# Optimization experiments

Hardware: AMD Instinct MI355X
Metric: run time of the kernel (lower is better)

## Reference

```python
import jax, jax.numpy as jnp
import numpy as np

N_QUBITS = 4
N_LAYERS = 2
_I2 = jnp.eye(2, dtype=jnp.complex64)
_X = jnp.array([[0.0, 1.0], [1.0, 0.0]], dtype=jnp.complex64)


def _apply_1q_batched(state, U, wire):
    # state: [B,2,2,2,2] complex, U: [B,2,2] (per-sample gate)
    s = jnp.moveaxis(state, 1 + wire, -1)
    s = jnp.einsum('bij,b...j->b...i', U, s)
    return jnp.moveaxis(s, -1, 1 + wire)


def _apply_1q(state, U, wire):
    # shared 2x2 gate on `wire`
    s = jnp.moveaxis(state, 1 + wire, -1)
    s = jnp.einsum('ij,...j->...i', U, s)
    return jnp.moveaxis(s, -1, 1 + wire)


def _apply_cnot(state, c, t):
    s = jnp.moveaxis(state, (1 + c, 1 + t), (-2, -1))  # [...,2(ctrl),2(tgt)]
    s = jnp.stack([s[..., 0, :], s[..., 1, ::-1]], axis=-2)  # flip target if ctrl=1
    return jnp.moveaxis(s, (-2, -1), (1 + c, 1 + t))


def _rot_matrix(phi, theta, omega):
    # qml.Rot = RZ(omega) @ RY(theta) @ RZ(phi)
    c, s = jnp.cos(theta / 2), jnp.sin(theta / 2)
    ep = jnp.exp(-0.5j * (phi + omega))  # e^{-i(phi+omega)/2}
    em = jnp.exp(-0.5j * (phi - omega))  # e^{-i(phi-omega)/2}
    return jnp.stack([
        jnp.stack([ep * c, -jnp.conj(em) * s]),
        jnp.stack([em * s, jnp.conj(ep) * c]),
    ]).astype(jnp.complex64)


def _circuit(angles, weights):
    # angles: [B, 4] real; weights: [2, 4, 3] real -> [B, 4] PauliZ expvals
    B = angles.shape[0]
    state = jnp.zeros((B,) + (2,) * N_QUBITS, jnp.complex64)
    state = state.at[(slice(None),) + (0,) * N_QUBITS].set(1.0)  # |0000>
    # AngleEmbedding (rotation='X'): RX(angle_w) on wire w, batched over samples
    for w in range(N_QUBITS):
        half = angles[:, w] / 2
        c, s = jnp.cos(half), jnp.sin(half)
        U = c[:, None, None] * _I2 - 1j * s[:, None, None] * _X  # [B,2,2]
        state = _apply_1q_batched(state, U, w)
    # StronglyEntanglingLayers: Rot on each wire, then ring of CNOTs with range r
    for l in range(N_LAYERS):
        for w in range(N_QUBITS):
            U = _rot_matrix(weights[l, w, 0], weights[l, w, 1], weights[l, w, 2])
            state = _apply_1q(state, U, w)
        r = (l % (N_QUBITS - 1)) + 1  # PennyLane default ranges
        for w in range(N_QUBITS):
            state = _apply_cnot(state, w, (w + r) % N_QUBITS)
    probs = state.real ** 2 + state.imag ** 2  # [B,2,2,2,2]
    z = []
    for w in range(N_QUBITS):
        other = tuple(a for a in range(1, N_QUBITS + 1) if a != 1 + w)
        p = probs.sum(other)  # [B,2]
        z.append(p[:, 0] - p[:, 1])
    return jnp.stack(z, axis=-1)  # [B,4]


def setup_inputs() -> dict:
    key = jax.random.key(0)
    ks = jax.random.split(key, 6)
    B, D_IN, D_OUT, NQ = 65536, 512, 512, N_QUBITS
    x = jax.random.normal(ks[0], (B, D_IN), jnp.float32)
    pre_W = jax.random.normal(ks[1], (NQ, D_IN), jnp.float32) / np.sqrt(D_IN)
    pre_b = jax.random.normal(ks[2], (NQ,), jnp.float32) * 0.05
    weights = jax.random.uniform(ks[3], (N_LAYERS, NQ, 3), jnp.float32) * (2 * np.pi)
    post_W = jax.random.normal(ks[4], (D_OUT, NQ), jnp.float32) / np.sqrt(NQ)
    post_b = jax.random.normal(ks[5], (D_OUT,), jnp.float32) * 0.05
    return {"x": x, "pre_W": pre_W, "pre_b": pre_b, "weights": weights,
            "post_W": post_W, "post_b": post_b}


def reference(x, pre_W, pre_b, weights, post_W, post_b):
    angles = jnp.tanh(x @ pre_W.T + pre_b) * jnp.pi  # [B,4]
    q = _circuit(angles, weights)                    # [B,4]
    return q @ post_W.T + post_b                     # [B,512]
```

## Files before the change

kernel.cpp:

```cpp
#include <hip/hip_runtime.h>
#include <math.h>

#define PI_F 3.14159265358979323846f


typedef float floatx4 __attribute__((ext_vector_type(4)));

static __device__ __forceinline__ void nt_store4(float* p, floatx4 v)
{
    __builtin_nontemporal_store(v, reinterpret_cast<floatx4*>(p));
}

static __device__ __forceinline__ float fast_tanh(float a)
{
    a = fminf(fmaxf(a, -15.f), 15.f);
    const float e = __expf(2.f * a);
    return (e - 1.f) / (e + 1.f);
}

template<int WIRE>
__device__ __forceinline__ void apply1q(float* sr, float* si,
    float u00r, float u00i, float u01r, float u01i,
    float u10r, float u10i, float u11r, float u11i)
{
    constexpr int st = 1 << (3 - WIRE);
#pragma unroll
    for (int i = 0; i < 16; ++i) {
        if (i & st) continue;
        const int j = i | st;
        const float r0 = sr[i], m0 = si[i], r1 = sr[j], m1 = si[j];
        sr[i] = u00r * r0 - u00i * m0 + u01r * r1 - u01i * m1;
        si[i] = u00r * m0 + u00i * r0 + u01r * m1 + u01i * r1;
        sr[j] = u10r * r0 - u10i * m0 + u11r * r1 - u11i * m1;
        si[j] = u10r * m0 + u10i * r0 + u11r * m1 + u11i * r1;
    }
}

template<int CW, int TW>
__device__ __forceinline__ void cnot(float* sr, float* si)
{
    constexpr int cb = 1 << (3 - CW), tb = 1 << (3 - TW);
#pragma unroll
    for (int i = 0; i < 16; ++i) {
        if ((i & cb) && !(i & tb)) {
            const int j = i | tb;
            float t;
            t = sr[i]; sr[i] = sr[j]; sr[j] = t;
            t = si[i]; si[i] = si[j]; si[j] = t;
        }
    }
}

#define APPLY_FAST(L, W) { \
    const float ph = wts[((L) * 4 + (W)) * 3 + 0]; \
    const float th = wts[((L) * 4 + (W)) * 3 + 1]; \
    const float om = wts[((L) * 4 + (W)) * 3 + 2]; \
    const float s_  = __sinf(0.5f * th),        c_  = __cosf(0.5f * th); \
    const float sp_ = __sinf(0.5f * (ph + om)), cp_ = __cosf(0.5f * (ph + om)); \
    const float sq_ = __sinf(0.5f * (ph - om)), cq_ = __cosf(0.5f * (ph - om)); \
    apply1q<W>(sr, si, cp_ * c_, -sp_ * c_, -cq_ * s_, -sq_ * s_, \
                       cq_ * s_, -sq_ * s_, cp_ * c_,  sp_ * c_); }

__global__ __launch_bounds__(256) void k_fused(
    const float* __restrict__ x,
    const float* __restrict__ preW,
    const float* __restrict__ preb,
    const float* __restrict__ wts,
    const float* __restrict__ postW,
    const float* __restrict__ postb,
    float* __restrict__ out, int B)
{
    const int lane  = threadIdx.x & 63;
    const int wid   = threadIdx.x >> 6;
    const int base  = blockIdx.x * 64;
    const int wbase = base + wid * 16;
    if (base >= B) return;

    __shared__ float4 angLds[64];

    float4 wA[4], wB[4];
#pragma unroll
    for (int w = 0; w < 4; ++w) {
        wA[w] = *reinterpret_cast<const float4*>(preW + w * 512 + lane * 4);
        wB[w] = *reinterpret_cast<const float4*>(preW + w * 512 + 256 + lane * 4);
    }
    const float4 pb = *reinterpret_cast<const float4*>(preb);

#pragma unroll
    for (int p = 0; p < 4; ++p) {
        const int b0 = wbase + p * 4;

        float4 xa[4], xb[4];
#pragma unroll
        for (int t = 0; t < 4; ++t) {
            const float* xr = x + (size_t)(b0 + t) * 512;
            xa[t] = *reinterpret_cast<const float4*>(xr + lane * 4);
            xb[t] = *reinterpret_cast<const float4*>(xr + 256 + lane * 4);
        }

        float acc[4][4];
#pragma unroll
        for (int t = 0; t < 4; ++t) {
#pragma unroll
            for (int w = 0; w < 4; ++w) {
                acc[t][w] = xa[t].x * wA[w].x + xa[t].y * wA[w].y + xa[t].z * wA[w].z + xa[t].w * wA[w].w
                          + xb[t].x * wB[w].x + xb[t].y * wB[w].y + xb[t].z * wB[w].z + xb[t].w * wB[w].w;
            }
        }

        float v[4];
#pragma unroll
        for (int t = 0; t < 4; ++t) {
            float a01 = (lane & 1) ? acc[t][1] : acc[t][0];
            float b01 = (lane & 1) ? acc[t][0] : acc[t][1];
            a01 += __shfl_xor(b01, 1, 64);
            float a23 = (lane & 1) ? acc[t][3] : acc[t][2];
            float b23 = (lane & 1) ? acc[t][2] : acc[t][3];
            a23 += __shfl_xor(b23, 1, 64);
            const float vv = (lane & 2) ? a23 : a01;
            const float uu = (lane & 2) ? a01 : a23;
            v[t] = vv + __shfl_xor(uu, 2, 64);
        }
        float c01 = (lane & 4) ? v[1] : v[0];
        float d01 = (lane & 4) ? v[0] : v[1];
        c01 += __shfl_xor(d01, 4, 64);
        float c23 = (lane & 4) ? v[3] : v[2];
        float d23 = (lane & 4) ? v[2] : v[3];
        c23 += __shfl_xor(d23, 4, 64);
        float m = (lane & 8) ? c23 : c01;
        float n = (lane & 8) ? c01 : c23;
        m += __shfl_xor(n, 8, 64);
        m += __shfl_xor(m, 16, 64);
        m += __shfl_xor(m, 32, 64);

        const float pb01 = (lane & 1) ? pb.y : pb.x;
        const float pb23 = (lane & 1) ? pb.w : pb.z;
        const float pbv  = (lane & 2) ? pb23 : pb01;
        const float angv = fast_tanh(m + pbv) * PI_F;

        if (lane < 16) {
            float* arow = reinterpret_cast<float*>(&angLds[wid * 16 + p * 4 + (lane >> 2)]);
            arow[lane & 3] = angv;
        }
    }

    __syncthreads();

    const int sid = lane >> 2;
    const float4 ang = angLds[wid * 16 + sid];

    const float s0 = __sinf(0.5f * ang.x), c0 = __cosf(0.5f * ang.x);
    const float s1 = __sinf(0.5f * ang.y), c1 = __cosf(0.5f * ang.y);
    const float s2 = __sinf(0.5f * ang.z), c2 = __cosf(0.5f * ang.z);
    const float s3 = __sinf(0.5f * ang.w), c3 = __cosf(0.5f * ang.w);

    float sr[16], si[16];
#pragma unroll
    for (int i = 0; i < 16; ++i) {
        const float r = ((i & 8) ? s0 : c0) * ((i & 4) ? s1 : c1)
                      * ((i & 2) ? s2 : c2) * ((i & 1) ? s3 : c3);
        const int mm = (((i >> 3) & 1) + ((i >> 2) & 1) + ((i >> 1) & 1) + (i & 1)) & 3;
        switch (mm) {
            case 0:  sr[i] = r;    si[i] = 0.f; break;
            case 1:  sr[i] = 0.f;  si[i] = -r;  break;
            case 2:  sr[i] = -r;   si[i] = 0.f; break;
            default: sr[i] = 0.f;  si[i] = r;   break;
        }
    }

    APPLY_FAST(0, 0); APPLY_FAST(0, 1); APPLY_FAST(0, 2); APPLY_FAST(0, 3);
    cnot<0, 1>(sr, si); cnot<1, 2>(sr, si); cnot<2, 3>(sr, si); cnot<3, 0>(sr, si);
    APPLY_FAST(1, 0); APPLY_FAST(1, 1); APPLY_FAST(1, 2); APPLY_FAST(1, 3);
    cnot<0, 2>(sr, si); cnot<1, 3>(sr, si); cnot<2, 0>(sr, si); cnot<3, 1>(sr, si);

    float z0 = 0.f, z1 = 0.f, z2 = 0.f, z3 = 0.f;
#pragma unroll
    for (int i = 0; i < 16; ++i) {
        const float p = sr[i] * sr[i] + si[i] * si[i];
        z0 += (i & 8) ? -p : p;
        z1 += (i & 4) ? -p : p;
        z2 += (i & 2) ? -p : p;
        z3 += (i & 1) ? -p : p;
    }

    const float4* pW4 = reinterpret_cast<const float4*>(postW);
    const float4* pb4 = reinterpret_cast<const float4*>(postb);
    const float4 p0 = pW4[4 * lane + 0], p1 = pW4[4 * lane + 1];
    const float4 p2 = pW4[4 * lane + 2], p3 = pW4[4 * lane + 3];
    const float4 p4 = pW4[4 * (64 + lane) + 0], p5 = pW4[4 * (64 + lane) + 1];
    const float4 p6 = pW4[4 * (64 + lane) + 2], p7 = pW4[4 * (64 + lane) + 3];
    const float4 bb0 = pb4[lane], bb1 = pb4[64 + lane];

#pragma unroll
    for (int s = 0; s < 16; ++s) {
        const float q0 = __shfl(z0, s * 4, 64);
        const float q1 = __shfl(z1, s * 4, 64);
        const float q2 = __shfl(z2, s * 4, 64);
        const float q3 = __shfl(z3, s * 4, 64);
        floatx4 o0, o1;
        o0.x = fmaf(q3, p0.w, fmaf(q2, p0.z, fmaf(q1, p0.y, fmaf(q0, p0.x, bb0.x))));
        o0.y = fmaf(q3, p1.w, fmaf(q2, p1.z, fmaf(q1, p1.y, fmaf(q0, p1.x, bb0.y))));
        o0.z = fmaf(q3, p2.w, fmaf(q2, p2.z, fmaf(q1, p2.y, fmaf(q0, p2.x, bb0.z))));
        o0.w = fmaf(q3, p3.w, fmaf(q2, p3.z, fmaf(q1, p3.y, fmaf(q0, p3.x, bb0.w))));
        o1.x = fmaf(q3, p4.w, fmaf(q2, p4.z, fmaf(q1, p4.y, fmaf(q0, p4.x, bb1.x))));
        o1.y = fmaf(q3, p5.w, fmaf(q2, p5.z, fmaf(q1, p5.y, fmaf(q0, p5.x, bb1.y))));
        o1.z = fmaf(q3, p6.w, fmaf(q2, p6.z, fmaf(q1, p6.y, fmaf(q0, p6.x, bb1.z))));
        o1.w = fmaf(q3, p7.w, fmaf(q2, p7.z, fmaf(q1, p7.y, fmaf(q0, p7.x, bb1.w))));
        float* orow = out + (size_t)(wbase + s) * 512;
        nt_store4(orow + 4 * lane, o0);
        nt_store4(orow + 256 + 4 * lane, o1);
    }
}

extern "C" void kernel_launch(void* const* d_in, const int* in_sizes, int n_in,
                              void* d_out, int out_size, void* d_ws, size_t ws_size,
                              hipStream_t stream)
{
    const float* x     = (const float*)d_in[0];
    const float* preW  = (const float*)d_in[1];
    const float* preb  = (const float*)d_in[2];
    const float* wts   = (const float*)d_in[3];
    const float* postW = (const float*)d_in[4];
    const float* postb = (const float*)d_in[5];
    float* out = (float*)d_out;
    const int B = in_sizes[0] / 512;

    k_fused<<<dim3((B + 63) / 64), dim3(256), 0, stream>>>(
        x, preW, preb, wts, postW, postb, out, B);
}
```

Baseline: 49.99 us.

## Double-buffer x loads across passes and process 32 rows per wave without LDS

Each wave now handles 32 rows in two tiles of 16, using a two-slot register buffer so the loads for the next 4-row pass are issued before the current pass's dot products and reductions. Angle redistribution moves from an LDS round-trip with __syncthreads to wave shuffles, which removes the block barrier. The grid is halved and each wave does twice the work. This hides HBM latency on the x reads and overlaps the quantum-circuit and output stores of the first tile with prefetches for the second, at the cost of higher register pressure and fewer waves in flight.

```diff
diff --git a/kernel.cpp b/kernel.cpp
--- a/kernel.cpp
+++ b/kernel.cpp
@@ -61,6 +61,55 @@
     apply1q<W>(sr, si, cp_ * c_, -sp_ * c_, -cq_ * s_, -sq_ * s_, \
                        cq_ * s_, -sq_ * s_, cp_ * c_,  sp_ * c_); }
 
+#define ISSUE_PASS(slot, p) { \
+    const float* xr_ = x + (size_t)(wbase + (p) * 4) * 512 + lane * 4; \
+    bxa[slot][0] = *reinterpret_cast<const float4*>(xr_); \
+    bxb[slot][0] = *reinterpret_cast<const float4*>(xr_ + 256); \
+    bxa[slot][1] = *reinterpret_cast<const float4*>(xr_ + 512); \
+    bxb[slot][1] = *reinterpret_cast<const float4*>(xr_ + 768); \
+    bxa[slot][2] = *reinterpret_cast<const float4*>(xr_ + 1024); \
+    bxb[slot][2] = *reinterpret_cast<const float4*>(xr_ + 1280); \
+    bxa[slot][3] = *reinterpret_cast<const float4*>(xr_ + 1536); \
+    bxb[slot][3] = *reinterpret_cast<const float4*>(xr_ + 1792); }
+
+#define DOTS_FOLD(slot, dest) { \
+    float acc[4][4]; \
+    _Pragma("unroll") \
+    for (int t = 0; t < 4; ++t) { \
+        _Pragma("unroll") \
+        for (int w = 0; w < 4; ++w) { \
+            acc[t][w] = bxa[slot][t].x * wA[w].x + bxa[slot][t].y * wA[w].y \
+                      + bxa[slot][t].z * wA[w].z + bxa[slot][t].w * wA[w].w \
+                      + bxb[slot][t].x * wB[w].x + bxb[slot][t].y * wB[w].y \
+                      + bxb[slot][t].z * wB[w].z + bxb[slot][t].w * wB[w].w; \
+        } \
+    } \
+    float v[4]; \
+    _Pragma("unroll") \
+    for (int t = 0; t < 4; ++t) { \
+        float a01 = (lane & 1) ? acc[t][1] : acc[t][0]; \
+        float b01 = (lane & 1) ? acc[t][0] : acc[t][1]; \
+        a01 += __shfl_xor(b01, 1, 64); \
+        float a23 = (lane & 1) ? acc[t][3] : acc[t][2]; \
+        float b23 = (lane & 1) ? acc[t][2] : acc[t][3]; \
+        a23 += __shfl_xor(b23, 1, 64); \
+        const float vv = (lane & 2) ? a23 : a01; \
+        const float uu = (lane & 2) ? a01 : a23; \
+        v[t] = vv + __shfl_xor(uu, 2, 64); \
+    } \
+    float c01 = (lane & 4) ? v[1] : v[0]; \
+    float d01 = (lane & 4) ? v[0] : v[1]; \
+    c01 += __shfl_xor(d01, 4, 64); \
+    float c23 = (lane & 4) ? v[3] : v[2]; \
+    float d23 = (lane & 4) ? v[2] : v[3]; \
+    c23 += __shfl_xor(d23, 4, 64); \
+    float m_ = (lane & 8) ? c23 : c01; \
+    float n_ = (lane & 8) ? c01 : c23; \
+    m_ += __shfl_xor(n_, 8, 64); \
+    m_ += __shfl_xor(m_, 16, 64); \
+    m_ += __shfl_xor(m_, 32, 64); \
+    dest = fast_tanh(m_ + pbv) * PI_F; }
+
 __global__ __launch_bounds__(256) void k_fused(
     const float* __restrict__ x,
     const float* __restrict__ preW,
@@ -72,11 +121,8 @@
 {
     const int lane  = threadIdx.x & 63;
     const int wid   = threadIdx.x >> 6;
-    const int base  = blockIdx.x * 64;
-    const int wbase = base + wid * 16;
-    if (base >= B) return;
-
-    __shared__ float4 angLds[64];
+    const int wbase = blockIdx.x * 128 + wid * 32;
+    if (wbase >= B) return;
 
     float4 wA[4], wB[4];
 #pragma unroll
@@ -85,131 +131,98 @@
         wB[w] = *reinterpret_cast<const float4*>(preW + w * 512 + 256 + lane * 4);
     }
     const float4 pb = *reinterpret_cast<const float4*>(preb);
-
-#pragma unroll
-    for (int p = 0; p < 4; ++p) {
-        const int b0 = wbase + p * 4;
-
-        float4 xa[4], xb[4];
-#pragma unroll
-        for (int t = 0; t < 4; ++t) {
-            const float* xr = x + (size_t)(b0 + t) * 512;
-            xa[t] = *reinterpret_cast<const float4*>(xr + lane * 4);
-            xb[t] = *reinterpret_cast<const float4*>(xr + 256 + lane * 4);
-        }
-
-        float acc[4][4];
-#pragma unroll
-        for (int t = 0; t < 4; ++t) {
-#pragma unroll
-            for (int w = 0; w < 4; ++w) {
-                acc[t][w] = xa[t].x * wA[w].x + xa[t].y * wA[w].y + xa[t].z * wA[w].z + xa[t].w * wA[w].w
-                          + xb[t].x * wB[w].x + xb[t].y * wB[w].y + xb[t].z * wB[w].z + xb[t].w * wB[w].w;
+    const float pb01 = (lane & 1) ? pb.y : pb.x;
+    const float pb23 = (lane & 1) ? pb.w : pb.z;
+    const float pbv  = (lane & 2) ? pb23 : pb01;
+
+    float4 bxa[2][4], bxb[2][4];
+
+    auto tile_body = [&](int tb, float a0, float a1, float a2, float a3) {
+        const float comb = (lane & 32) ? ((lane & 16) ? a3 : a2)
+                                       : ((lane & 16) ? a1 : a0);
+        const int sb = (lane & 48) + 4 * ((lane >> 2) & 3);
+        const float A0 = __shfl(comb, sb + 0, 64);
+        const float A1 = __shfl(comb, sb + 1, 64);
+        const float A2 = __shfl(comb, sb + 2, 64);
+        const float A3 = __shfl(comb, sb + 3, 64);
+
+        const float4* pW4 = reinterpret_cast<const float4*>(postW);
+        const float4* pb4 = reinterpret_cast<const float4*>(postb);
+        const float4 p0 = pW4[4 * lane + 0], p1 = pW4[4 * lane + 1];
+        const float4 p2 = pW4[4 * lane + 2], p3 = pW4[4 * lane + 3];
+        const float4 p4 = pW4[4 * (64 + lane) + 0], p5 = pW4[4 * (64 + lane) + 1];
+        const float4 p6 = pW4[4 * (64 + lane) + 2], p7 = pW4[4 * (64 + lane) + 3];
+        const float4 bb0 = pb4[lane], bb1 = pb4[64 + lane];
+
+        const float s0 = __sinf(0.5f * A0), c0 = __cosf(0.5f * A0);
+        const float s1 = __sinf(0.5f * A1), c1 = __cosf(0.5f * A1);
+        const float s2 = __sinf(0.5f * A2), c2 = __cosf(0.5f * A2);
+        const float s3 = __sinf(0.5f * A3), c3 = __cosf(0.5f * A3);
+
+        float sr[16], si[16];
+#pragma unroll
+        for (int i = 0; i < 16; ++i) {
+            const float r = ((i & 8) ? s0 : c0) * ((i & 4) ? s1 : c1)
+                          * ((i & 2) ? s2 : c2) * ((i & 1) ? s3 : c3);
+            const int mm = (((i >> 3) & 1) + ((i >> 2) & 1) + ((i >> 1) & 1) + (i & 1)) & 3;
+            switch (mm) {
+                case 0:  sr[i] = r;    si[i] = 0.f; break;
+                case 1:  sr[i] = 0.f;  si[i] = -r;  break;
+                case 2:  sr[i] = -r;   si[i] = 0.f; break;
+                default: sr[i] = 0.f;  si[i] = r;   break;
             }
         }
 
-        float v[4];
-#pragma unroll
-        for (int t = 0; t < 4; ++t) {
-            float a01 = (lane & 1) ? acc[t][1] : acc[t][0];
-            float b01 = (lane & 1) ? acc[t][0] : acc[t][1];
-            a01 += __shfl_xor(b01, 1, 64);
-            float a23 = (lane & 1) ? acc[t][3] : acc[t][2];
-            float b23 = (lane & 1) ? acc[t][2] : acc[t][3];
-            a23 += __shfl_xor(b23, 1, 64);
-            const float vv = (lane & 2) ? a23 : a01;
-            const float uu = (lane & 2) ? a01 : a23;
-            v[t] = vv + __shfl_xor(uu, 2, 64);
-        }
-        float c01 = (lane & 4) ? v[1] : v[0];
-        float d01 = (lane & 4) ? v[0] : v[1];
-        c01 += __shfl_xor(d01, 4, 64);
-        float c23 = (lane & 4) ? v[3] : v[2];
-        float d23 = (lane & 4) ? v[2] : v[3];
-        c23 += __shfl_xor(d23, 4, 64);
-        float m = (lane & 8) ? c23 : c01;
-        float n = (lane & 8) ? c01 : c23;
-        m += __shfl_xor(n, 8, 64);
-        m += __shfl_xor(m, 16, 64);
-        m += __shfl_xor(m, 32, 64);
-
-        const float pb01 = (lane & 1) ? pb.y : pb.x;
-        const float pb23 = (lane & 1) ? pb.w : pb.z;
-        const float pbv  = (lane & 2) ? pb23 : pb01;
-        const float angv = fast_tanh(m + pbv) * PI_F;
-
-        if (lane < 16) {
-            float* arow = reinterpret_cast<float*>(&angLds[wid * 16 + p * 4 + (lane >> 2)]);
-            arow[lane & 3] = angv;
-        }
-    }
-
-    __syncthreads();
-
-    const int sid = lane >> 2;
-    const float4 ang = angLds[wid * 16 + sid];
-
-    const float s0 = __sinf(0.5f * ang.x), c0 = __cosf(0.5f * ang.x);
-    const float s1 = __sinf(0.5f * ang.y), c1 = __cosf(0.5f * ang.y);
-    const float s2 = __sinf(0.5f * ang.z), c2 = __cosf(0.5f * ang.z);
-    const float s3 = __sinf(0.5f * ang.w), c3 = __cosf(0.5f * ang.w);
-
-    float sr[16], si[16];
-#pragma unroll
-    for (int i = 0; i < 16; ++i) {
-        const float r = ((i & 8) ? s0 : c0) * ((i & 4) ? s1 : c1)
-                      * ((i & 2) ? s2 : c2) * ((i & 1) ? s3 : c3);
-        const int mm = (((i >> 3) & 1) + ((i >> 2) & 1) + ((i >> 1) & 1) + (i & 1)) & 3;
-        switch (mm) {
-            case 0:  sr[i] = r;    si[i] = 0.f; break;
-            case 1:  sr[i] = 0.f;  si[i] = -r;  break;
-            case 2:  sr[i] = -r;   si[i] = 0.f; break;
-            default: sr[i] = 0.f;  si[i] = r;   break;
-        }
-    }
-
-    APPLY_FAST(0, 0); APPLY_FAST(0, 1); APPLY_FAST(0, 2); APPLY_FAST(0, 3);
-    cnot<0, 1>(sr, si); cnot<1, 2>(sr, si); cnot<2, 3>(sr, si); cnot<3, 0>(sr, si);
-    APPLY_FAST(1, 0); APPLY_FAST(1, 1); APPLY_FAST(1, 2); APPLY_FAST(1, 3);
-    cnot<0, 2>(sr, si); cnot<1, 3>(sr, si); cnot<2, 0>(sr, si); cnot<3, 1>(sr, si);
-
-    float z0 = 0.f, z1 = 0.f, z2 = 0.f, z3 = 0.f;
-#pragma unroll
-    for (int i = 0; i < 16; ++i) {
-        const float p = sr[i] * sr[i] + si[i] * si[i];
-        z0 += (i & 8) ? -p : p;
-        z1 += (i & 4) ? -p : p;
-        z2 += (i & 2) ? -p : p;
-        z3 += (i & 1) ? -p : p;
-    }
-
-    const float4* pW4 = reinterpret_cast<const float4*>(postW);
-    const float4* pb4 = reinterpret_cast<const float4*>(postb);
-    const float4 p0 = pW4[4 * lane + 0], p1 = pW4[4 * lane + 1];
-    const float4 p2 = pW4[4 * lane + 2], p3 = pW4[4 * lane + 3];
-    const float4 p4 = pW4[4 * (64 + lane) + 0], p5 = pW4[4 * (64 + lane) + 1];
-    const float4 p6 = pW4[4 * (64 + lane) + 2], p7 = pW4[4 * (64 + lane) + 3];
-    const float4 bb0 = pb4[lane], bb1 = pb4[64 + lane];
-
-#pragma unroll
-    for (int s = 0; s < 16; ++s) {
-        const float q0 = __shfl(z0, s * 4, 64);
-        const float q1 = __shfl(z1, s * 4, 64);
-        const float q2 = __shfl(z2, s * 4, 64);
-        const float q3 = __shfl(z3, s * 4, 64);
-        floatx4 o0, o1;
-        o0.x = fmaf(q3, p0.w, fmaf(q2, p0.z, fmaf(q1, p0.y, fmaf(q0, p0.x, bb0.x))));
-        o0.y = fmaf(q3, p1.w, fmaf(q2, p1.z, fmaf(q1, p1.y, fmaf(q0, p1.x, bb0.y))));
-        o0.z = fmaf(q3, p2.w, fmaf(q2, p2.z, fmaf(q1, p2.y, fmaf(q0, p2.x, bb0.z))));
-        o0.w = fmaf(q3, p3.w, fmaf(q2, p3.z, fmaf(q1, p3.y, fmaf(q0, p3.x, bb0.w))));
-        o1.x = fmaf(q3, p4.w, fmaf(q2, p4.z, fmaf(q1, p4.y, fmaf(q0, p4.x, bb1.x))));
-        o1.y = fmaf(q3, p5.w, fmaf(q2, p5.z, fmaf(q1, p5.y, fmaf(q0, p5.x, bb1.y))));
-        o1.z = fmaf(q3, p6.w, fmaf(q2, p6.z, fmaf(q1, p6.y, fmaf(q0, p6.x, bb1.z))));
-        o1.w = fmaf(q3, p7.w, fmaf(q2, p7.z, fmaf(q1, p7.y, fmaf(q0, p7.x, bb1.w))));
-        float* orow = out + (size_t)(wbase + s) * 512;
-        nt_store4(orow + 4 * lane, o0);
-        nt_store4(orow + 256 + 4 * lane, o1);
-    }
+        APPLY_FAST(0, 0); APPLY_FAST(0, 1); APPLY_FAST(0, 2); APPLY_FAST(0, 3);
+        cnot<0, 1>(sr, si); cnot<1, 2>(sr, si); cnot<2, 3>(sr, si); cnot<3, 0>(sr, si);
+        APPLY_FAST(1, 0); APPLY_FAST(1, 1); APPLY_FAST(1, 2); APPLY_FAST(1, 3);
+        cnot<0, 2>(sr, si); cnot<1, 3>(sr, si); cnot<2, 0>(sr, si); cnot<3, 1>(sr, si);
+
+        float z0 = 0.f, z1 = 0.f, z2 = 0.f, z3 = 0.f;
+#pragma unroll
+        for (int i = 0; i < 16; ++i) {
+            const float p = sr[i] * sr[i] + si[i] * si[i];
+            z0 += (i & 8) ? -p : p;
+            z1 += (i & 4) ? -p : p;
+            z2 += (i & 2) ? -p : p;
+            z3 += (i & 1) ? -p : p;
+        }
+
+#pragma unroll
+        for (int s = 0; s < 16; ++s) {
+            const float q0 = __shfl(z0, s * 4, 64);
+            const float q1 = __shfl(z1, s * 4, 64);
+            const float q2 = __shfl(z2, s * 4, 64);
+            const float q3 = __shfl(z3, s * 4, 64);
+            floatx4 o0, o1;
+            o0.x = fmaf(q3, p0.w, fmaf(q2, p0.z, fmaf(q1, p0.y, fmaf(q0, p0.x, bb0.x))));
+            o0.y = fmaf(q3, p1.w, fmaf(q2, p1.z, fmaf(q1, p1.y, fmaf(q0, p1.x, bb0.y))));
+            o0.z = fmaf(q3, p2.w, fmaf(q2, p2.z, fmaf(q1, p2.y, fmaf(q0, p2.x, bb0.z))));
+            o0.w = fmaf(q3, p3.w, fmaf(q2, p3.z, fmaf(q1, p3.y, fmaf(q0, p3.x, bb0.w))));
+            o1.x = fmaf(q3, p4.w, fmaf(q2, p4.z, fmaf(q1, p4.y, fmaf(q0, p4.x, bb1.x))));
+            o1.y = fmaf(q3, p5.w, fmaf(q2, p5.z, fmaf(q1, p5.y, fmaf(q0, p5.x, bb1.y))));
+            o1.z = fmaf(q3, p6.w, fmaf(q2, p6.z, fmaf(q1, p6.y, fmaf(q0, p6.x, bb1.z))));
+            o1.w = fmaf(q3, p7.w, fmaf(q2, p7.z, fmaf(q1, p7.y, fmaf(q0, p7.x, bb1.w))));
+            float* orow = out + (size_t)(tb + s) * 512;
+            nt_store4(orow + 4 * lane, o0);
+            nt_store4(orow + 256 + 4 * lane, o1);
+        }
+    };
+
+    float a0, a1, a2, a3;
+
+    ISSUE_PASS(0, 0);
+    ISSUE_PASS(1, 1);
+    DOTS_FOLD(0, a0);  ISSUE_PASS(0, 2);
+    DOTS_FOLD(1, a1);  ISSUE_PASS(1, 3);
+    DOTS_FOLD(0, a2);  ISSUE_PASS(0, 4);
+    DOTS_FOLD(1, a3);  ISSUE_PASS(1, 5);
+    tile_body(wbase, a0, a1, a2, a3);
+    DOTS_FOLD(0, a0);  ISSUE_PASS(0, 6);
+    DOTS_FOLD(1, a1);  ISSUE_PASS(1, 7);
+    DOTS_FOLD(0, a2);
+    DOTS_FOLD(1, a3);
+    tile_body(wbase + 16, a0, a1, a2, a3);
 }
 
 extern "C" void kernel_launch(void* const* d_in, const int* in_sizes, int n_in,
@@ -225,6 +238,6 @@
     float* out = (float*)d_out;
     const int B = in_sizes[0] / 512;
 
-    k_fused<<<dim3((B + 63) / 64), dim3(256), 0, stream>>>(
+    k_fused<<<dim3((B + 127) / 128), dim3(256), 0, stream>>>(
         x, preW, preb, wts, postW, postb, out, B);
 }
```

New measurement: 55.23 us. 1.1x slower.
